# Performance work log

Hardware: AMD Instinct MI355X
Metric: run time of the kernel (lower is better)

## Reference

```python
import jax, jax.numpy as jnp
import numpy as np

NH = 8  # num_heads
EPS_LN = 1e-5
BN_DENOM = float(np.sqrt(1.0 + 1e-5))  # eval-mode BN with running_mean=0, running_var=1


def _layernorm(x, g, b):
    m = jnp.mean(x, axis=-1, keepdims=True)
    v = jnp.var(x, axis=-1, keepdims=True)
    return (x - m) * jax.lax.rsqrt(v + EPS_LN) * g + b


def _rope(q, k):
    # q,k: [B, H, T, D]
    t, d = q.shape[2], q.shape[3]
    half = d // 2
    pos = jnp.arange(t, dtype=q.dtype)[:, None]
    idx = jnp.arange(half, dtype=q.dtype)[None, :]
    inv_freq = 1.0 / (10000.0 ** (idx / half))
    ang = pos * inv_freq  # [T, half]
    sin = jnp.sin(ang)[None, None]
    cos = jnp.cos(ang)[None, None]

    def rot(x):
        x1, x2 = x[..., :half], x[..., half:]
        return jnp.concatenate([x1 * cos - x2 * sin, x1 * sin + x2 * cos], axis=-1)

    return rot(q), rot(k)


def _sep_conv(y, dw, pw):
    # y: [B, C, T]; dw: [C, 1, K]; pw: [O, C]
    c = y.shape[1]
    k = dw.shape[-1]
    y = jax.lax.conv_general_dilated(
        y, dw, window_strides=(2,), padding=[(k // 2, k // 2)],
        dimension_numbers=('NCH', 'OIH', 'NCH'), feature_group_count=c)
    return jnp.einsum('bct,oc->bot', y, pw)


def _attn(h, Wq, bq, Wk, bk, Wv, bv, Wo, bo):
    b, t, e = h.shape
    hd = e // NH
    scale = hd ** -0.5

    def split(z):
        return jnp.transpose(z.reshape(b, t, NH, hd), (0, 2, 1, 3))

    q = split(h @ Wq.T + bq)
    k = split(h @ Wk.T + bk)
    v = split(h @ Wv.T + bv)
    q, k = _rope(q, k)
    logits = jnp.einsum('bhtd,bhsd->bhts', q, k) * scale
    attn = jax.nn.softmax(logits, axis=-1)
    ctx = jnp.einsum('bhts,bhsd->bhtd', attn, v)
    ctx = jnp.transpose(ctx, (0, 2, 1, 3)).reshape(b, t, e)
    return ctx @ Wo.T + bo


def setup_inputs() -> dict:
    key = jax.random.key(0)
    ks = jax.random.split(key, 40)
    B, T, Cin = 8, 4096, 64
    E, L, MLP = 256, 6, 1024
    s = 0.02
    p = {}
    p['x'] = jax.random.normal(ks[0], (B, T, Cin), jnp.float32)
    p['conv1_dw'] = jax.random.normal(ks[1], (Cin, 1, 7), jnp.float32) * s
    p['conv1_pw'] = jax.random.normal(ks[2], (64, Cin), jnp.float32) * s
    p['bn1_g'] = jnp.ones((64,), jnp.float32)
    p['bn1_b'] = jnp.zeros((64,), jnp.float32)
    p['conv2_dw'] = jax.random.normal(ks[3], (64, 1, 7), jnp.float32) * s
    p['conv2_pw'] = jax.random.normal(ks[4], (128, 64), jnp.float32) * s
    p['bn2_g'] = jnp.ones((128,), jnp.float32)
    p['bn2_b'] = jnp.zeros((128,), jnp.float32)
    p['proj_w'] = jax.random.normal(ks[5], (E, 128), jnp.float32) * s
    p['proj_b'] = jnp.zeros((E,), jnp.float32)
    p['cls_tok'] = jax.random.normal(ks[6], (1, 1, E), jnp.float32) * s
    p['Wq'] = jax.random.normal(ks[7], (L, E, E), jnp.float32) * s
    p['bq'] = jnp.zeros((L, E), jnp.float32)
    p['Wk'] = jax.random.normal(ks[8], (L, E, E), jnp.float32) * s
    p['bk'] = jnp.zeros((L, E), jnp.float32)
    p['Wv'] = jax.random.normal(ks[9], (L, E, E), jnp.float32) * s
    p['bv'] = jnp.zeros((L, E), jnp.float32)
    p['Wo'] = jax.random.normal(ks[10], (L, E, E), jnp.float32) * s
    p['bo'] = jnp.zeros((L, E), jnp.float32)
    p['ln1_g'] = jnp.ones((L, E), jnp.float32)
    p['ln1_b'] = jnp.zeros((L, E), jnp.float32)
    p['mlp_w1'] = jax.random.normal(ks[11], (L, MLP, E), jnp.float32) * s
    p['mlp_b1'] = jnp.zeros((L, MLP), jnp.float32)
    p['mlp_w2'] = jax.random.normal(ks[12], (L, E, MLP), jnp.float32) * s
    p['mlp_b2'] = jnp.zeros((L, E), jnp.float32)
    p['ln2_g'] = jnp.ones((L, E), jnp.float32)
    p['ln2_b'] = jnp.zeros((L, E), jnp.float32)
    p['lat_w'] = jax.random.normal(ks[13], (E, E), jnp.float32) * s
    p['lat_b'] = jnp.zeros((E,), jnp.float32)
    p['latn_g'] = jnp.ones((E,), jnp.float32)
    p['latn_b'] = jnp.zeros((E,), jnp.float32)
    p['ts_w'] = jax.random.normal(ks[14], (1, E), jnp.float32) * s
    p['ts_b'] = jnp.zeros((1,), jnp.float32)
    return p


def reference(x, conv1_dw, conv1_pw, bn1_g, bn1_b, conv2_dw, conv2_pw, bn2_g, bn2_b,
              proj_w, proj_b, cls_tok, Wq, bq, Wk, bk, Wv, bv, Wo, bo,
              ln1_g, ln1_b, mlp_w1, mlp_b1, mlp_w2, mlp_b2, ln2_g, ln2_b,
              lat_w, lat_b, latn_g, latn_b, ts_w, ts_b):
    B = x.shape[0]
    y = jnp.transpose(x, (0, 2, 1))  # [B, C, T]
    y = _sep_conv(y, conv1_dw, conv1_pw)
    y = (y / BN_DENOM) * bn1_g[None, :, None] + bn1_b[None, :, None]
    y = jax.nn.gelu(y, approximate=False)
    y = _sep_conv(y, conv2_dw, conv2_pw)
    y = (y / BN_DENOM) * bn2_g[None, :, None] + bn2_b[None, :, None]
    y = jax.nn.gelu(y, approximate=False)
    y = jnp.transpose(y, (0, 2, 1))  # [B, T', 128]
    h = y @ proj_w.T + proj_b  # [B, T', E]
    h = jnp.concatenate([jnp.broadcast_to(cls_tok, (B, 1, h.shape[-1])), h], axis=1)
    L = Wq.shape[0]
    for i in range(L):
        a = _attn(h, Wq[i], bq[i], Wk[i], bk[i], Wv[i], bv[i], Wo[i], bo[i])
        h = _layernorm(h + a, ln1_g[i], ln1_b[i])
        m = jax.nn.gelu(h @ mlp_w1[i].T + mlp_b1[i], approximate=False) @ mlp_w2[i].T + mlp_b2[i]
        h = _layernorm(h + m, ln2_g[i], ln2_b[i])
    h = _layernorm(h @ lat_w.T + lat_b, latn_g, latn_b)
    logits = h[:, 1:] @ ts_w.T + ts_b  # per-time-step logits (CLS excluded)
    return logits
```

## Files before the change

### kernel.cpp

```cpp
#include <hip/hip_runtime.h>
#include <hip/hip_bf16.h>
#include <math.h>

typedef __hip_bfloat16 bf16;
typedef __attribute__((ext_vector_type(8))) short bf16x8_t;
typedef __attribute__((ext_vector_type(4))) short bf16x4_t;
typedef __attribute__((ext_vector_type(4))) float f32x4_t;

#define BN_RDENOM 0.9999950000374997f
#define EPS_LN 1e-5f
#define ATTN_SCALE 0.17677669529663687f
#define S_LEN 1025
#define S_PAD 1088
#define E_DIM 256
#define NHEAD 8
#define HDIM 32
#define MROWS (8 * S_LEN)
#define WSLOT 786432

__device__ __forceinline__ float bf(const bf16 v) { return __bfloat162float(v); }
__device__ __forceinline__ bf16 tobf(float v) { return __float2bfloat16(v); }
__device__ __forceinline__ short bfbits(float v) {
    bf16 t = __float2bfloat16(v); short s; __builtin_memcpy(&s, &t, 2); return s;
}
__device__ __forceinline__ float gelu_exact(float x) {
    return 0.5f * x * (1.0f + erff(x * 0.70710678118654752f));
}

#define DPP_ROR(x, N) __int_as_float(__builtin_amdgcn_update_dpp(0, __float_as_int(x), 0x120 + (N), 0xF, 0xF, false))
__device__ __forceinline__ float row_allsum(float x) {
    x = x + DPP_ROR(x, 1);
    x = x + DPP_ROR(x, 2);
    x = x + DPP_ROR(x, 4);
    x = x + DPP_ROR(x, 8);
    return x;
}

__global__ __launch_bounds__(256) void cvt_w(const float* __restrict__ src,
    bf16* __restrict__ dst, int n)
{
    int i = (blockIdx.x * 256 + threadIdx.x) * 4;
    if (i >= n) return;
    f32x4_t v = *(const f32x4_t*)(src + i);
    bf16x4_t o;
    #pragma unroll
    for (int j = 0; j < 4; ++j) o[j] = bfbits(v[j]);
    *(bf16x4_t*)((short*)dst + i) = o;
}

__global__ __launch_bounds__(256) void cvt_layer6(const float* __restrict__ wq,
    const float* __restrict__ wk, const float* __restrict__ wv, const float* __restrict__ wo,
    const float* __restrict__ w1, const float* __restrict__ w2, bf16* __restrict__ dst)
{
    int l = blockIdx.y;
    int i = (blockIdx.x * 256 + threadIdx.x) * 4;
    const float* s; int off;
    if (i < 262144) {
        s = (i < 65536) ? wq : (i < 131072) ? wk : (i < 196608) ? wv : wo;
        s += (size_t)l * 65536;
        off = i & 65535;
    } else if (i < 524288) { s = w1 + (size_t)l * 262144; off = i - 262144; }
    else                   { s = w2 + (size_t)l * 262144; off = i - 524288; }
    f32x4_t v = *(const f32x4_t*)(s + off);
    bf16x4_t o;
    #pragma unroll
    for (int j = 0; j < 4; ++j) o[j] = bfbits(v[j]);
    *(bf16x4_t*)((short*)dst + (size_t)l * WSLOT + i) = o;
}

__global__ __launch_bounds__(256) void conv_sep1(const float* __restrict__ x,
    const float* __restrict__ dw, const float* __restrict__ pw,
    const float* __restrict__ g, const float* __restrict__ bb,
    bf16* __restrict__ out)
{
    __shared__ float xs[70][64];
    __shared__ float dy[32][64];
    __shared__ float pws[64][65];
    __shared__ float dws[64][7];
    int blk = blockIdx.x;
    int tile = blk & 63, b = blk >> 6;
    int t0 = tile * 32;
    int tid = threadIdx.x;
    int tbase = t0 * 2 - 3;
    for (int i = tid; i < 70 * 64; i += 256) {
        int r = i >> 6, c = i & 63;
        int t = tbase + r;
        xs[r][c] = (t >= 0 && t < 4096) ? x[((size_t)b * 4096 + t) * 64 + c] : 0.f;
    }
    for (int i = tid; i < 64 * 7; i += 256) dws[i / 7][i % 7] = dw[i];
    for (int i = tid; i < 64 * 64; i += 256) pws[i >> 6][i & 63] = pw[i];
    __syncthreads();
    for (int i = tid; i < 32 * 64; i += 256) {
        int tl = i >> 6, c = i & 63;
        float s = 0.f;
        #pragma unroll
        for (int j = 0; j < 7; ++j) s += xs[2 * tl + j][c] * dws[c][j];
        dy[tl][c] = s;
    }
    __syncthreads();
    for (int i = tid; i < 32 * 64; i += 256) {
        int tl = i >> 6, o = i & 63;
        float s = 0.f;
        #pragma unroll 8
        for (int c = 0; c < 64; ++c) s += dy[tl][c] * pws[o][c];
        s = s * BN_RDENOM * g[o] + bb[o];
        out[((size_t)(b * 2048 + t0 + tl)) * 64 + o] = tobf(gelu_exact(s));
    }
}

__global__ __launch_bounds__(256) void conv_sep2(const bf16* __restrict__ x,
    const float* __restrict__ dw, const float* __restrict__ pw,
    const float* __restrict__ g, const float* __restrict__ bb,
    bf16* __restrict__ out)
{
    __shared__ float xs[70][64];
    __shared__ float dy[32][64];
    __shared__ float pws[128][65];
    __shared__ float dws[64][7];
    int blk = blockIdx.x;
    int tile = blk & 31, b = blk >> 5;
    int t0 = tile * 32;
    int tid = threadIdx.x;
    int tbase = t0 * 2 - 3;
    for (int i = tid; i < 70 * 64; i += 256) {
        int r = i >> 6, c = i & 63;
        int t = tbase + r;
        xs[r][c] = (t >= 0 && t < 2048) ? bf(x[((size_t)b * 2048 + t) * 64 + c]) : 0.f;
    }
    for (int i = tid; i < 64 * 7; i += 256) dws[i / 7][i % 7] = dw[i];
    for (int i = tid; i < 128 * 64; i += 256) pws[i >> 6][i & 63] = pw[i];
    __syncthreads();
    for (int i = tid; i < 32 * 64; i += 256) {
        int tl = i >> 6, c = i & 63;
        float s = 0.f;
        #pragma unroll
        for (int j = 0; j < 7; ++j) s += xs[2 * tl + j][c] * dws[c][j];
        dy[tl][c] = s;
    }
    __syncthreads();
    for (int i = tid; i < 32 * 128; i += 256) {
        int tl = i >> 7, o = i & 127;
        float s = 0.f;
        #pragma unroll 8
        for (int c = 0; c < 64; ++c) s += dy[tl][c] * pws[o][c];
        s = s * BN_RDENOM * g[o] + bb[o];
        out[((size_t)(b * 1024 + t0 + tl)) * 128 + o] = tobf(gelu_exact(s));
    }
}

template <int ACT>
__global__ __launch_bounds__(256) void gemm_bf(const bf16* __restrict__ A,
    const bf16* __restrict__ W, const float* __restrict__ bias,
    bf16* __restrict__ C, int M, int N, int K)
{
    __shared__ short As[64 * 72];
    __shared__ short Bs[64 * 72];
    int tid = threadIdx.x;
    int wave = tid >> 6, lane = tid & 63, quad = lane >> 4, l16 = lane & 15;
    int wm = wave & 1, wn = wave >> 1;
    int m0 = blockIdx.x * 64, n0 = blockIdx.y * 64;

    f32x4_t zero4 = {0.f, 0.f, 0.f, 0.f};
    f32x4_t acc[2][2];
    acc[0][0] = zero4; acc[0][1] = zero4; acc[1][0] = zero4; acc[1][1] = zero4;

    int srow = tid >> 2, skc = (tid & 3) * 16;
    for (int k0 = 0; k0 < K; k0 += 64) {
        {
            int m = m0 + srow;
            bf16x8_t a0 = {}, a1 = {};
            if (m < M) {
                a0 = *(const bf16x8_t*)(A + (size_t)m * K + k0 + skc);
                a1 = *(const bf16x8_t*)(A + (size_t)m * K + k0 + skc + 8);
            }
            *(bf16x8_t*)(&As[srow * 72 + skc])     = a0;
            *(bf16x8_t*)(&As[srow * 72 + skc + 8]) = a1;
        }
        {
            const bf16* wp = W + (size_t)(n0 + srow) * K + k0 + skc;
            *(bf16x8_t*)(&Bs[srow * 72 + skc])     = *(const bf16x8_t*)(wp);
            *(bf16x8_t*)(&Bs[srow * 72 + skc + 8]) = *(const bf16x8_t*)(wp + 8);
        }
        __syncthreads();
        #pragma unroll
        for (int ks = 0; ks < 2; ++ks) {
            bf16x8_t a[2], b[2];
            #pragma unroll
            for (int mi = 0; mi < 2; ++mi)
                a[mi] = *(bf16x8_t*)(&As[(wm * 32 + mi * 16 + l16) * 72 + ks * 32 + quad * 8]);
            #pragma unroll
            for (int ni = 0; ni < 2; ++ni)
                b[ni] = *(bf16x8_t*)(&Bs[(wn * 32 + ni * 16 + l16) * 72 + ks * 32 + quad * 8]);
            #pragma unroll
            for (int mi = 0; mi < 2; ++mi)
                #pragma unroll
                for (int ni = 0; ni < 2; ++ni)
                    acc[mi][ni] = __builtin_amdgcn_mfma_f32_16x16x32_bf16(a[mi], b[ni], acc[mi][ni], 0, 0, 0);
        }
        __syncthreads();
    }
    #pragma unroll
    for (int mi = 0; mi < 2; ++mi) {
        #pragma unroll
        for (int ni = 0; ni < 2; ++ni) {
            int col = n0 + wn * 32 + ni * 16 + l16;
            float bv = bias[col];
            #pragma unroll
            for (int r = 0; r < 4; ++r) {
                int row = m0 + wm * 32 + mi * 16 + quad * 4 + r;
                if (row < M) {
                    float v = acc[mi][ni][r] + bv;
                    if (ACT == 1) v = gelu_exact(v);
                    C[(size_t)row * N + col] = tobf(v);
                }
            }
        }
    }
}

template <int ACT>
__global__ __launch_bounds__(256) void gemm_bf128(const bf16* __restrict__ A,
    const bf16* __restrict__ W, const float* __restrict__ bias,
    bf16* __restrict__ C, int M, int N, int K)
{
    __shared__ short As[128 * 72];
    __shared__ short Bs[64 * 72];
    int tid = threadIdx.x;
    int wave = tid >> 6, lane = tid & 63, quad = lane >> 4, l16 = lane & 15;
    int wm = wave & 1, wn = wave >> 1;
    int m0 = blockIdx.x * 128, n0 = blockIdx.y * 64;

    f32x4_t zero4 = {0.f, 0.f, 0.f, 0.f};
    f32x4_t acc[4][2];
    #pragma unroll
    for (int i = 0; i < 4; ++i) { acc[i][0] = zero4; acc[i][1] = zero4; }

    int srow = tid >> 2, skc = (tid & 3) * 16;
    for (int k0 = 0; k0 < K; k0 += 64) {
        #pragma unroll
        for (int p = 0; p < 2; ++p) {
            int row = srow + p * 64;
            int m = m0 + row;
            bf16x8_t a0 = {}, a1 = {};
            if (m < M) {
                a0 = *(const bf16x8_t*)(A + (size_t)m * K + k0 + skc);
                a1 = *(const bf16x8_t*)(A + (size_t)m * K + k0 + skc + 8);
            }
            *(bf16x8_t*)(&As[row * 72 + skc])     = a0;
            *(bf16x8_t*)(&As[row * 72 + skc + 8]) = a1;
        }
        {
            const bf16* wp = W + (size_t)(n0 + srow) * K + k0 + skc;
            *(bf16x8_t*)(&Bs[srow * 72 + skc])     = *(const bf16x8_t*)(wp);
            *(bf16x8_t*)(&Bs[srow * 72 + skc + 8]) = *(const bf16x8_t*)(wp + 8);
        }
        __syncthreads();
        #pragma unroll
        for (int ks = 0; ks < 2; ++ks) {
            bf16x8_t a[4], b[2];
            #pragma unroll
            for (int mi = 0; mi < 4; ++mi)
                a[mi] = *(bf16x8_t*)(&As[(wm * 64 + mi * 16 + l16) * 72 + ks * 32 + quad * 8]);
            #pragma unroll
            for (int ni = 0; ni < 2; ++ni)
                b[ni] = *(bf16x8_t*)(&Bs[(wn * 32 + ni * 16 + l16) * 72 + ks * 32 + quad * 8]);
            #pragma unroll
            for (int mi = 0; mi < 4; ++mi)
                #pragma unroll
                for (int ni = 0; ni < 2; ++ni)
                    acc[mi][ni] = __builtin_amdgcn_mfma_f32_16x16x32_bf16(a[mi], b[ni], acc[mi][ni], 0, 0, 0);
        }
        __syncthreads();
    }
    #pragma unroll
    for (int mi = 0; mi < 4; ++mi) {
        #pragma unroll
        for (int ni = 0; ni < 2; ++ni) {
            int col = n0 + wn * 32 + ni * 16 + l16;
            float bv = bias[col];
            #pragma unroll
            for (int r = 0; r < 4; ++r) {
                int row = m0 + wm * 64 + mi * 16 + quad * 4 + r;
                if (row < M) {
                    float v = acc[mi][ni][r] + bv;
                    if (ACT == 1) v = gelu_exact(v);
                    C[(size_t)row * N + col] = tobf(v);
                }
            }
        }
    }
}

__global__ __launch_bounds__(256) void gemm_qkv128(const bf16* __restrict__ A,
    const bf16* __restrict__ Wqkv, const float* __restrict__ bq,
    const float* __restrict__ bk, const float* __restrict__ bv,
    bf16* __restrict__ qo, bf16* __restrict__ ko, bf16* __restrict__ vo, int M)
{
    const int K = 256, N = 256;
    __shared__ short As[128 * 72];
    __shared__ short Bs[64 * 72];
    int part = blockIdx.y >> 2;
    int n0 = (blockIdx.y & 3) * 64;
    const bf16* W     = Wqkv + (size_t)part * 65536;
    const float* bias = (part == 0) ? bq : (part == 1) ? bk : bv;
    bf16* C           = (part == 0) ? qo : (part == 1) ? ko : vo;
    bool dorope = (part < 2);
    float oscale = (part == 0) ? ATTN_SCALE : 1.0f;

    int tid = threadIdx.x;
    int wave = tid >> 6, lane = tid & 63, quad = lane >> 4, l16 = lane & 15;
    int wm = wave & 1, wn = wave >> 1;
    int m0 = blockIdx.x * 128;

    f32x4_t zero4 = {0.f, 0.f, 0.f, 0.f};
    f32x4_t acc[4][2];
    #pragma unroll
    for (int i = 0; i < 4; ++i) { acc[i][0] = zero4; acc[i][1] = zero4; }

    int srow = tid >> 2, skc = (tid & 3) * 16;
    for (int k0 = 0; k0 < K; k0 += 64) {
        #pragma unroll
        for (int p = 0; p < 2; ++p) {
            int row = srow + p * 64;
            int m = m0 + row;
            bf16x8_t a0 = {}, a1 = {};
            if (m < M) {
                a0 = *(const bf16x8_t*)(A + (size_t)m * K + k0 + skc);
                a1 = *(const bf16x8_t*)(A + (size_t)m * K + k0 + skc + 8);
            }
            *(bf16x8_t*)(&As[row * 72 + skc])     = a0;
            *(bf16x8_t*)(&As[row * 72 + skc + 8]) = a1;
        }
        {
            const bf16* wp = W + (size_t)(n0 + srow) * K + k0 + skc;
            *(bf16x8_t*)(&Bs[srow * 72 + skc])     = *(const bf16x8_t*)(wp);
            *(bf16x8_t*)(&Bs[srow * 72 + skc + 8]) = *(const bf16x8_t*)(wp + 8);
        }
        __syncthreads();
        #pragma unroll
        for (int ks = 0; ks < 2; ++ks) {
            bf16x8_t a[4], b[2];
            #pragma unroll
            for (int mi = 0; mi < 4; ++mi)
                a[mi] = *(bf16x8_t*)(&As[(wm * 64 + mi * 16 + l16) * 72 + ks * 32 + quad * 8]);
            #pragma unroll
            for (int ni = 0; ni < 2; ++ni)
                b[ni] = *(bf16x8_t*)(&Bs[(wn * 32 + ni * 16 + l16) * 72 + ks * 32 + quad * 8]);
            #pragma unroll
            for (int mi = 0; mi < 4; ++mi)
                #pragma unroll
                for (int ni = 0; ni < 2; ++ni)
                    acc[mi][ni] = __builtin_amdgcn_mfma_f32_16x16x32_bf16(a[mi], b[ni], acc[mi][ni], 0, 0, 0);
        }
        __syncthreads();
    }
    int col0 = n0 + wn * 32 + l16;
    float b1v = bias[col0], b2v = bias[col0 + 16];
    float invf = powf(10000.f, -(float)l16 * (1.f / 16.f));
    #pragma unroll
    for (int mi = 0; mi < 4; ++mi) {
        #pragma unroll
        for (int r = 0; r < 4; ++r) {
            int row = m0 + wm * 64 + mi * 16 + quad * 4 + r;
            if (row >= M) continue;
            int bb = row / S_LEN, t = row - bb * S_LEN;
            float x1 = acc[mi][0][r] + b1v;
            float x2 = acc[mi][1][r] + b2v;
            if (dorope) {
                float ang = (float)t * invf;
                float sn, cs;
                __sincosf(ang, &sn, &cs);
                float y1 = (x1 * cs - x2 * sn) * oscale;
                float y2 = (x1 * sn + x2 * cs) * oscale;
                x1 = y1; x2 = y2;
            }
            size_t obase = ((size_t)bb * S_PAD + t) * N;
            C[obase + col0]      = tobf(x1);
            C[obase + col0 + 16] = tobf(x2);
        }
    }
}

__global__ __launch_bounds__(256) void assemble_h(const bf16* __restrict__ tmp,
    const float* __restrict__ cls, bf16* __restrict__ h)
{
    int row = blockIdx.x;
    int tid = threadIdx.x;
    int b = row / S_LEN, t = row % S_LEN;
    bf16 v = (t == 0) ? tobf(cls[tid]) : tmp[((size_t)(b * 1024 + t - 1)) * E_DIM + tid];
    h[(size_t)row * E_DIM + tid] = v;
}

__global__ __launch_bounds__(256) void attn_mfma(const bf16* __restrict__ Q,
    const bf16* __restrict__ K, const bf16* __restrict__ V, bf16* __restrict__ O)
{
    __shared__ short VTs[2][32 * 72];
    __shared__ short Ps[4][16 * 72];
    int blk = blockIdx.x;
    int bh = blk & 63;
    int qt = blk >> 6;
    int hh = bh & 7, b = bh >> 3;
    int tid = threadIdx.x;
    int wave = tid >> 6, lane = tid & 63, quad = lane >> 4, l16 = lane & 15;
    int q0 = qt * 64 + wave * 16;
    const size_t bSp = (size_t)b * S_PAD;
    const size_t bS  = (size_t)b * S_LEN;
    const size_t hoff = (size_t)hh * HDIM;
    const bf16* Qb = Q + bSp * E_DIM + hoff;
    const bf16* Kb = K + bSp * E_DIM + hoff;
    const bf16* Vb = V + bSp * E_DIM + hoff;

    f32x4_t zero4 = {0.f, 0.f, 0.f, 0.f};
    bf16x8_t qfrag = *(const bf16x8_t*)(Qb + (size_t)(q0 + l16) * E_DIM + quad * 8);
    f32x4_t o0 = zero4, o1 = zero4;
    float lsum[4] = {0.f, 0.f, 0.f, 0.f};

    int vs = tid >> 2, vd = (tid & 3) * 8;
    short* myP = Ps[wave];

    bf16x8_t vpre = *(const bf16x8_t*)(Vb + (size_t)vs * E_DIM + vd);

    for (int c = 0; c < 17; ++c) {
        int s0 = c * 64;
        short* VT = VTs[c & 1];
        #pragma unroll
        for (int j = 0; j < 8; ++j) VT[(vd + j) * 72 + vs] = vpre[j];
        if (c < 16)
            vpre = *(const bf16x8_t*)(Vb + (size_t)(s0 + 64 + vs) * E_DIM + vd);
        f32x4_t sc[4];
        #pragma unroll
        for (int kk = 0; kk < 4; ++kk) {
            bf16x8_t kf = *(const bf16x8_t*)(Kb + (size_t)(s0 + kk * 16 + l16) * E_DIM + quad * 8);
            sc[kk] = __builtin_amdgcn_mfma_f32_16x16x32_bf16(qfrag, kf, zero4, 0, 0, 0);
        }
        #pragma unroll
        for (int r = 0; r < 4; ++r) {
            float ps = 0.f;
            #pragma unroll
            for (int kk = 0; kk < 4; ++kk) {
                int s = s0 + kk * 16 + l16;
                float raw = (s < S_LEN) ? sc[kk][r] : -1e30f;
                float p = __expf(raw);
                ps += p;
                myP[(quad * 4 + r) * 72 + kk * 16 + l16] = bfbits(p);
            }
            lsum[r] += ps;
        }
        __syncthreads();
        #pragma unroll
        for (int half = 0; half < 2; ++half) {
            int off = half * 32 + quad * 8;
            bf16x8_t pf  = *(bf16x8_t*)(&myP[l16 * 72 + off]);
            bf16x8_t vf0 = *(bf16x8_t*)(&VT[l16 * 72 + off]);
            bf16x8_t vf1 = *(bf16x8_t*)(&VT[(16 + l16) * 72 + off]);
            o0 = __builtin_amdgcn_mfma_f32_16x16x32_bf16(pf, vf0, o0, 0, 0, 0);
            o1 = __builtin_amdgcn_mfma_f32_16x16x32_bf16(pf, vf1, o1, 0, 0, 0);
        }
    }
    #pragma unroll
    for (int r = 0; r < 4; ++r) {
        int qrow = q0 + quad * 4 + r;
        if (qrow < S_LEN) {
            float rs = 1.f / row_allsum(lsum[r]);
            O[(bS + qrow) * E_DIM + hoff + l16]      = tobf(o0[r] * rs);
            O[(bS + qrow) * E_DIM + hoff + 16 + l16] = tobf(o1[r] * rs);
        }
    }
}

__global__ __launch_bounds__(256) void ln_kernel(const bf16* __restrict__ X,
    const bf16* __restrict__ R, const float* __restrict__ g,
    const float* __restrict__ b, bf16* __restrict__ out)
{
    int wave = threadIdx.x >> 6, lane = threadIdx.x & 63;
    int row0 = blockIdx.x * 8 + wave * 2;
    size_t base0 = (size_t)row0 * E_DIM + lane * 4;
    size_t base1 = base0 + E_DIM;
    float v0[4], v1[4];
    {
        bf16x4_t xa = *(const bf16x4_t*)(X + base0);
        bf16x4_t xb = *(const bf16x4_t*)(X + base1);
        #pragma unroll
        for (int i = 0; i < 4; ++i) {
            bf16 t; short s;
            s = xa[i]; __builtin_memcpy(&t, &s, 2); v0[i] = bf(t);
            s = xb[i]; __builtin_memcpy(&t, &s, 2); v1[i] = bf(t);
        }
    }
    if (R) {
        bf16x4_t ra = *(const bf16x4_t*)(R + base0);
        bf16x4_t rb = *(const bf16x4_t*)(R + base1);
        #pragma unroll
        for (int i = 0; i < 4; ++i) {
            bf16 t; short s;
            s = ra[i]; __builtin_memcpy(&t, &s, 2); v0[i] += bf(t);
            s = rb[i]; __builtin_memcpy(&t, &s, 2); v1[i] += bf(t);
        }
    }
    float s0 = v0[0] + v0[1] + v0[2] + v0[3];
    float s1 = v1[0] + v1[1] + v1[2] + v1[3];
    #pragma unroll
    for (int off = 32; off; off >>= 1) { s0 += __shfl_xor(s0, off); s1 += __shfl_xor(s1, off); }
    float m0 = s0 * (1.f / 256.f), m1 = s1 * (1.f / 256.f);
    float w0 = 0.f, w1 = 0.f;
    #pragma unroll
    for (int i = 0; i < 4; ++i) {
        v0[i] -= m0; w0 += v0[i] * v0[i];
        v1[i] -= m1; w1 += v1[i] * v1[i];
    }
    #pragma unroll
    for (int off = 32; off; off >>= 1) { w0 += __shfl_xor(w0, off); w1 += __shfl_xor(w1, off); }
    float r0 = rsqrtf(w0 * (1.f / 256.f) + EPS_LN);
    float r1 = rsqrtf(w1 * (1.f / 256.f) + EPS_LN);
    int c = lane * 4;
    bf16x4_t oa, ob;
    #pragma unroll
    for (int i = 0; i < 4; ++i) {
        oa[i] = bfbits(v0[i] * r0 * g[c + i] + b[c + i]);
        ob[i] = bfbits(v1[i] * r1 * g[c + i] + b[c + i]);
    }
    *(bf16x4_t*)(out + base0) = oa;
    *(bf16x4_t*)(out + base1) = ob;
}

__global__ __launch_bounds__(256) void ts_kernel(const bf16* __restrict__ H,
    const float* __restrict__ w, const float* __restrict__ tb,
    float* __restrict__ out)
{
    int wid = (blockIdx.x << 2) + (threadIdx.x >> 6);
    int lane = threadIdx.x & 63;
    int b = wid >> 10, t = wid & 1023;
    const bf16* row = H + ((size_t)(b * S_LEN + t + 1)) * E_DIM;
    float acc = 0.f;
    for (int e = lane; e < E_DIM; e += 64) acc += bf(row[e]) * w[e];
    #pragma unroll
    for (int off = 32; off; off >>= 1) acc += __shfl_down(acc, off, 64);
    if (lane == 0) out[wid] = acc + tb[0];
}

extern "C" void kernel_launch(void* const* d_in, const int* in_sizes, int n_in,
                              void* d_out, int out_size, void* d_ws, size_t ws_size,
                              hipStream_t stream)
{
    (void)in_sizes; (void)n_in; (void)out_size; (void)ws_size;
    const float* X        = (const float*)d_in[0];
    const float* CONV1_DW = (const float*)d_in[1];
    const float* CONV1_PW = (const float*)d_in[2];
    const float* BN1_G    = (const float*)d_in[3];
    const float* BN1_B    = (const float*)d_in[4];
    const float* CONV2_DW = (const float*)d_in[5];
    const float* CONV2_PW = (const float*)d_in[6];
    const float* BN2_G    = (const float*)d_in[7];
    const float* BN2_B    = (const float*)d_in[8];
    const float* PROJ_W   = (const float*)d_in[9];
    const float* PROJ_B   = (const float*)d_in[10];
    const float* CLS      = (const float*)d_in[11];
    const float* WQ       = (const float*)d_in[12];
    const float* BQ       = (const float*)d_in[13];
    const float* WK       = (const float*)d_in[14];
    const float* BK       = (const float*)d_in[15];
    const float* WV       = (const float*)d_in[16];
    const float* BV       = (const float*)d_in[17];
    const float* WO       = (const float*)d_in[18];
    const float* BO       = (const float*)d_in[19];
    const float* LN1G     = (const float*)d_in[20];
    const float* LN1B     = (const float*)d_in[21];
    const float* W1       = (const float*)d_in[22];
    const float* B1       = (const float*)d_in[23];
    const float* W2       = (const float*)d_in[24];
    const float* B2       = (const float*)d_in[25];
    const float* LN2G     = (const float*)d_in[26];
    const float* LN2B     = (const float*)d_in[27];
    const float* LATW     = (const float*)d_in[28];
    const float* LATB     = (const float*)d_in[29];
    const float* LATNG    = (const float*)d_in[30];
    const float* LATNB    = (const float*)d_in[31];
    const float* TSW      = (const float*)d_in[32];
    const float* TSB      = (const float*)d_in[33];

    const size_t SROW  = (size_t)MROWS * E_DIM;
    const size_t SPROW = (size_t)8 * S_PAD * E_DIM;
    bf16* h    = (bf16*)d_ws;
    bf16* bufB = h + SROW;
    bf16* r0   = bufB + SROW;
    bf16* q  = r0;
    bf16* k  = r0 + SPROW;
    bf16* v  = r0 + 2 * SPROW;
    bf16* cx = r0 + 3 * SPROW;
    bf16* wall = cx + SROW;
    bf16* pslot = wall + 6 * WSLOT;
    bf16* y1 = r0;
    bf16* y2 = r0 + SROW;
    bf16* mid = r0;

    conv_sep1<<<dim3(512), dim3(256), 0, stream>>>(X, CONV1_DW, CONV1_PW, BN1_G, BN1_B, y1);
    conv_sep2<<<dim3(256), dim3(256), 0, stream>>>(y1, CONV2_DW, CONV2_PW, BN2_G, BN2_B, y2);
    cvt_w<<<dim3(32), dim3(256), 0, stream>>>(PROJ_W, pslot, 32768);
    gemm_bf<0><<<dim3(128, 4), dim3(256), 0, stream>>>(y2, pslot, PROJ_B, bufB, 8192, 256, 128);
    assemble_h<<<dim3(MROWS), dim3(256), 0, stream>>>(bufB, CLS, h);
    cvt_layer6<<<dim3(768, 6), dim3(256), 0, stream>>>(WQ, WK, WV, WO, W1, W2, wall);

    for (int l = 0; l < 6; ++l) {
        bf16* wslot = wall + (size_t)l * WSLOT;
        gemm_qkv128<<<dim3(65, 12), dim3(256), 0, stream>>>(h, wslot,
            BQ + l * 256, BK + l * 256, BV + l * 256, q, k, v, MROWS);
        attn_mfma<<<dim3(64 * 17), dim3(256), 0, stream>>>(q, k, v, cx);
        gemm_bf<0><<<dim3(129, 4), dim3(256), 0, stream>>>(cx, wslot + 196608, BO + l * 256, bufB, MROWS, 256, 256);
        ln_kernel<<<dim3(MROWS / 8), dim3(256), 0, stream>>>(h, bufB, LN1G + l * 256, LN1B + l * 256, h);
        gemm_bf128<1><<<dim3(65, 16), dim3(256), 0, stream>>>(h, wslot + 262144, B1 + l * 1024, mid, MROWS, 1024, 256);
        gemm_bf<0><<<dim3(129, 4), dim3(256), 0, stream>>>(mid, wslot + 524288, B2 + l * 256, bufB, MROWS, 256, 1024);
        ln_kernel<<<dim3(MROWS / 8), dim3(256), 0, stream>>>(h, bufB, LN2G + l * 256, LN2B + l * 256, h);
    }

    cvt_w<<<dim3(64), dim3(256), 0, stream>>>(LATW, pslot, 65536);
    gemm_bf<0><<<dim3(129, 4), dim3(256), 0, stream>>>(h, pslot, LATB, bufB, MROWS, 256, 256);
    ln_kernel<<<dim3(MROWS / 8), dim3(256), 0, stream>>>(bufB, nullptr, LATNG, LATNB, r0);
    ts_kernel<<<dim3(2048), dim3(256), 0, stream>>>(r0, TSW, TSB, (float*)d_out);
}
```

Before: 835.8 us.

## Split attention over key halves with a separate combine kernel

Each attention block now processes only half of the key/value chunks, so the grid doubles. Unnormalized partial outputs and per-row exp sums are written out per half. A new combine kernel adds the two partials and divides by the total sum. This raises parallelism at the cost of extra global memory traffic, an extra launch per layer, and bf16 rounding of the unnormalized partials.

Result: slower. 883.9 us (+5.8%).

```diff
diff --git a/kernel.cpp b/kernel.cpp
--- a/kernel.cpp
+++ b/kernel.cpp
@@ -392,13 +392,15 @@
 }
 
 __global__ __launch_bounds__(256) void attn_mfma(const bf16* __restrict__ Q,
-    const bf16* __restrict__ K, const bf16* __restrict__ V, bf16* __restrict__ O)
+    const bf16* __restrict__ K, const bf16* __restrict__ V,
+    bf16* __restrict__ PO, float* __restrict__ LS)
 {
     __shared__ short VTs[2][32 * 72];
     __shared__ short Ps[4][16 * 72];
     int blk = blockIdx.x;
     int bh = blk & 63;
-    int qt = blk >> 6;
+    int r2 = blk >> 6;
+    int qt = r2 >> 1, sh = r2 & 1;
     int hh = bh & 7, b = bh >> 3;
     int tid = threadIdx.x;
     int wave = tid >> 6, lane = tid & 63, quad = lane >> 4, l16 = lane & 15;
@@ -409,6 +411,7 @@
     const bf16* Qb = Q + bSp * E_DIM + hoff;
     const bf16* Kb = K + bSp * E_DIM + hoff;
     const bf16* Vb = V + bSp * E_DIM + hoff;
+    int c0 = sh ? 9 : 0, c1 = sh ? 17 : 9;
 
     f32x4_t zero4 = {0.f, 0.f, 0.f, 0.f};
     bf16x8_t qfrag = *(const bf16x8_t*)(Qb + (size_t)(q0 + l16) * E_DIM + quad * 8);
@@ -418,14 +421,14 @@
     int vs = tid >> 2, vd = (tid & 3) * 8;
     short* myP = Ps[wave];
 
-    bf16x8_t vpre = *(const bf16x8_t*)(Vb + (size_t)vs * E_DIM + vd);
-
-    for (int c = 0; c < 17; ++c) {
+    bf16x8_t vpre = *(const bf16x8_t*)(Vb + (size_t)(c0 * 64 + vs) * E_DIM + vd);
+
+    for (int c = c0; c < c1; ++c) {
         int s0 = c * 64;
         short* VT = VTs[c & 1];
         #pragma unroll
         for (int j = 0; j < 8; ++j) VT[(vd + j) * 72 + vs] = vpre[j];
-        if (c < 16)
+        if (c + 1 < c1)
             vpre = *(const bf16x8_t*)(Vb + (size_t)(s0 + 64 + vs) * E_DIM + vd);
         f32x4_t sc[4];
         #pragma unroll
@@ -457,15 +460,44 @@
             o1 = __builtin_amdgcn_mfma_f32_16x16x32_bf16(pf, vf1, o1, 0, 0, 0);
         }
     }
+    bf16* POb = PO + (size_t)sh * ((size_t)MROWS * E_DIM);
     #pragma unroll
     for (int r = 0; r < 4; ++r) {
         int qrow = q0 + quad * 4 + r;
         if (qrow < S_LEN) {
-            float rs = 1.f / row_allsum(lsum[r]);
-            O[(bS + qrow) * E_DIM + hoff + l16]      = tobf(o0[r] * rs);
-            O[(bS + qrow) * E_DIM + hoff + 16 + l16] = tobf(o1[r] * rs);
-        }
-    }
+            float lt = row_allsum(lsum[r]);
+            POb[(bS + qrow) * E_DIM + hoff + l16]      = tobf(o0[r]);
+            POb[(bS + qrow) * E_DIM + hoff + 16 + l16] = tobf(o1[r]);
+            if (l16 == 0)
+                LS[((size_t)(sh * 64 + bh)) * S_PAD + qrow] = lt;
+        }
+    }
+}
+
+__global__ __launch_bounds__(256) void attn_combine(const bf16* __restrict__ PO,
+    const float* __restrict__ LS, bf16* __restrict__ O)
+{
+    int row = blockIdx.x * 4 + (threadIdx.x >> 6);
+    int lane = threadIdx.x & 63;
+    int b = row / S_LEN, t = row - b * S_LEN;
+    int hh = lane >> 3;
+    int bh = b * 8 + hh;
+    float l0 = LS[(size_t)bh * S_PAD + t];
+    float l1 = LS[(size_t)(64 + bh) * S_PAD + t];
+    float rs = 1.f / (l0 + l1);
+    size_t base = (size_t)row * E_DIM + lane * 4;
+    const size_t HALF = (size_t)MROWS * E_DIM;
+    bf16x4_t a = *(const bf16x4_t*)(PO + base);
+    bf16x4_t c = *(const bf16x4_t*)(PO + HALF + base);
+    bf16x4_t o;
+    #pragma unroll
+    for (int i = 0; i < 4; ++i) {
+        bf16 ta, tc; short s;
+        s = a[i]; __builtin_memcpy(&ta, &s, 2);
+        s = c[i]; __builtin_memcpy(&tc, &s, 2);
+        o[i] = bfbits((bf(ta) + bf(tc)) * rs);
+    }
+    *(bf16x4_t*)(O + base) = o;
 }
 
 __global__ __launch_bounds__(256) void ln_kernel(const bf16* __restrict__ X,
@@ -589,6 +621,8 @@
     bf16* cx = r0 + 3 * SPROW;
     bf16* wall = cx + SROW;
     bf16* pslot = wall + 6 * WSLOT;
+    bf16* po = pslot + 65536;
+    float* ls = (float*)(po + 2 * SROW);
     bf16* y1 = r0;
     bf16* y2 = r0 + SROW;
     bf16* mid = r0;
@@ -604,7 +638,8 @@
         bf16* wslot = wall + (size_t)l * WSLOT;
         gemm_qkv128<<<dim3(65, 12), dim3(256), 0, stream>>>(h, wslot,
             BQ + l * 256, BK + l * 256, BV + l * 256, q, k, v, MROWS);
-        attn_mfma<<<dim3(64 * 17), dim3(256), 0, stream>>>(q, k, v, cx);
+        attn_mfma<<<dim3(64 * 34), dim3(256), 0, stream>>>(q, k, v, po, ls);
+        attn_combine<<<dim3(MROWS / 4), dim3(256), 0, stream>>>(po, ls, cx);
         gemm_bf<0><<<dim3(129, 4), dim3(256), 0, stream>>>(cx, wslot + 196608, BO + l * 256, bufB, MROWS, 256, 256);
         ln_kernel<<<dim3(MROWS / 8), dim3(256), 0, stream>>>(h, bufB, LN1G + l * 256, LN1B + l * 256, h);
         gemm_bf128<1><<<dim3(65, 16), dim3(256), 0, stream>>>(h, wslot + 262144, B1 + l * 1024, mid, MROWS, 1024, 256);
```
